# Optimization experiments

Measured on AMD Instinct MI355X. Metric: run time of the kernel, lower is better.

Reference implementation:

```python
import jax, jax.numpy as jnp
import numpy as np
import math

EPS = 1e-5
HEADS = 8

def _lin(x, w, b):
    return x @ w.T + b

def _ln(x, g, b):
    m = x.mean(-1, keepdims=True)
    v = ((x - m) ** 2).mean(-1, keepdims=True)
    return (x - m) / jnp.sqrt(v + EPS) * g + b

def _bn_eval(x, g, b):
    # BatchNorm1d eval with init running stats (mean=0, var=1)
    return x / jnp.sqrt(1.0 + EPS) * g[None, :, None] + b[None, :, None]

def _conv1d(x, w, b, pad):
    y = jax.lax.conv_general_dilated(x, w, (1,), [(pad, pad)],
                                     dimension_numbers=('NCH', 'OIH', 'NCH'))
    return y + b[None, :, None]

def _interp_linear(x, out_len):
    # F.interpolate(mode='linear', align_corners=False) on last axis
    L = x.shape[-1]
    src = (jnp.arange(out_len) + 0.5) * (L / out_len) - 0.5
    src = jnp.clip(src, 0.0, L - 1)
    i0 = jnp.floor(src).astype(jnp.int32)
    i1 = jnp.minimum(i0 + 1, L - 1)
    w = (src - i0).astype(x.dtype)
    return x[..., i0] * (1.0 - w) + x[..., i1] * w

def setup_inputs():
    key = jax.random.key(0)
    ks = iter(jax.random.split(key, 64))
    def nrm(shape, scale=0.02):
        return jax.random.normal(next(ks), shape, dtype=jnp.float32) * scale
    B, T, N, H, HOR, C = 2, 64, 2048, 128, 24, 32
    return dict(
        x=jax.random.normal(next(ks), (B, T, N), dtype=jnp.float32),
        tc_w=nrm((C, 1, 3), 0.2), tc_b=jnp.zeros((C,)), tc_bn_g=jnp.ones((C,)), tc_bn_b=jnp.zeros((C,)),
        fp_w=nrm((H, C * T)), fp_b=jnp.zeros((H,)), fp_ln_g=jnp.ones((H,)), fp_ln_b=jnp.zeros((H,)),
        q_w=nrm((H, H)), q_b=jnp.zeros((H,)),
        k_w=nrm((H, H)), k_b=jnp.zeros((H,)),
        v_w=nrm((H, H)), v_b=jnp.zeros((H,)),
        o_w=nrm((H, H)), o_b=jnp.zeros((H,)),
        adj=nrm((1, HEADS, N, N), 0.02),
        s0_w=nrm((H, H, 1), 0.05), s0_b=jnp.zeros((H,)), s0_bn_g=jnp.ones((H,)), s0_bn_b=jnp.zeros((H,)),
        s1_w=nrm((H, H, 2), 0.05), s1_b=jnp.zeros((H,)), s1_bn_g=jnp.ones((H,)), s1_bn_b=jnp.zeros((H,)),
        fusion_weight=jnp.ones((2,)),
        fu_w=nrm((H, H)), fu_b=jnp.zeros((H,)), fu_ln_g=jnp.ones((H,)), fu_ln_b=jnp.zeros((H,)),
        pr1_w=nrm((H, H)), pr1_b=jnp.zeros((H,)), pr_ln_g=jnp.ones((H,)), pr_ln_b=jnp.zeros((H,)),
        pr2_w=nrm((HOR, H)), pr2_b=jnp.zeros((HOR,)),
        rg_w=nrm((HOR, H)), rg_b=jnp.zeros((HOR,)),
    )

def _forward(x, tc_w, tc_b, tc_bn_g, tc_bn_b, fp_w, fp_b, fp_ln_g, fp_ln_b,
             q_w, q_b, k_w, k_b, v_w, v_b, o_w, o_b, adj,
             s0_w, s0_b, s0_bn_g, s0_bn_b, s1_w, s1_b, s1_bn_g, s1_bn_b,
             fusion_weight, fu_w, fu_b, fu_ln_g, fu_ln_b,
             pr1_w, pr1_b, pr_ln_g, pr_ln_b, pr2_w, pr2_b, rg_w, rg_b):
    B, T, N = x.shape
    H = q_w.shape[0]
    hd = H // HEADS
    x_last = x[:, -1, :]                                  # (B, N)
    # temporal conv over the window per node
    xt = x.transpose(0, 2, 1).reshape(B * N, 1, T)
    f = jax.nn.relu(_bn_eval(_conv1d(xt, tc_w, tc_b, 1), tc_bn_g, tc_bn_b))
    f = f.reshape(B, N, -1)                               # (B, N, 32*T)
    feats = jax.nn.relu(_ln(_lin(f, fp_w, fp_b), fp_ln_g, fp_ln_b))
    # adaptive graph attention with learnable adjacency bias
    q = _lin(feats, q_w, q_b).reshape(B, N, HEADS, hd)
    k = _lin(feats, k_w, k_b).reshape(B, N, HEADS, hd)
    v = _lin(feats, v_w, v_b).reshape(B, N, HEADS, hd)
    scores = jnp.einsum('bnhd,bmhd->bhnm', q, k) / math.sqrt(hd) + adj
    attn = jax.nn.softmax(scores, axis=-1)                # (B, HEADS, N, N)
    reg = jnp.float32(1e-4) * jnp.mean(jnp.abs(attn))
    go = jnp.einsum('bhnm,bmhd->bnhd', attn, v).reshape(B, N, H)
    gf = _lin(go, o_w, o_b)                               # (B, N, H)
    # multi-scale fusion (conv over node axis, kernels 1 and 2)
    xc = gf.transpose(0, 2, 1)                            # (B, H, N)
    f0 = jax.nn.relu(_bn_eval(_conv1d(xc, s0_w, s0_b, 0), s0_bn_g, s0_bn_b))
    f1 = jax.nn.relu(_bn_eval(_conv1d(xc, s1_w, s1_b, 1), s1_bn_g, s1_bn_b))  # (B,H,N+1)
    f1 = _interp_linear(f1, N)
    alpha = jax.nn.softmax(fusion_weight)
    fused = (alpha[0] * f0 + alpha[1] * f1).transpose(0, 2, 1)
    ff = jax.nn.relu(_ln(_lin(fused, fu_w, fu_b), fu_ln_g, fu_ln_b))
    # progressive prediction refinement
    h = jax.nn.relu(_ln(_lin(ff, pr1_w, pr1_b), pr_ln_g, pr_ln_b))
    preds = _lin(h, pr2_w, pr2_b)                         # (B, N, horizon)
    gates = jax.nn.sigmoid(_lin(ff, rg_w, rg_b))
    refined = gates * x_last[..., None] + (1.0 - gates) * preds
    return refined.transpose(0, 2, 1), reg                # (B, horizon, N), scalar

def reference(x, tc_w, tc_b, tc_bn_g, tc_bn_b, fp_w, fp_b, fp_ln_g, fp_ln_b,
              q_w, q_b, k_w, k_b, v_w, v_b, o_w, o_b, adj,
              s0_w, s0_b, s0_bn_g, s0_bn_b, s1_w, s1_b, s1_bn_g, s1_bn_b,
              fusion_weight, fu_w, fu_b, fu_ln_g, fu_ln_b,
              pr1_w, pr1_b, pr_ln_g, pr_ln_b, pr2_w, pr2_b, rg_w, rg_b):
    return _forward(x, tc_w, tc_b, tc_bn_g, tc_bn_b, fp_w, fp_b, fp_ln_g, fp_ln_b,
                    q_w, q_b, k_w, k_b, v_w, v_b, o_w, o_b, adj,
                    s0_w, s0_b, s0_bn_g, s0_bn_b, s1_w, s1_b, s1_bn_g, s1_bn_b,
                    fusion_weight, fu_w, fu_b, fu_ln_g, fu_ln_b,
                    pr1_w, pr1_b, pr_ln_g, pr_ln_b, pr2_w, pr2_b, rg_w, rg_b)
```

## Files before the change

### kernel.cpp

```cpp
#include <hip/hip_runtime.h>

using f32x4  = __attribute__((ext_vector_type(4))) float;
using bf16x8 = __attribute__((ext_vector_type(8))) short;

#define DEV static __device__ __forceinline__

DEV unsigned short f2bf(float f){
  unsigned u = __float_as_uint(f);
  unsigned r = (u + 0x7FFFu + ((u >> 16) & 1u)) >> 16;
  return (unsigned short)r;
}

__global__ __launch_bounds__(256) void prep_conv_kernel(
    const float* __restrict__ fp_w, const float* __restrict__ q_w,
    const float* __restrict__ k_w, const float* __restrict__ v_w,
    const float* __restrict__ o_w, const float* __restrict__ s0_w,
    const float* __restrict__ s1_w, const float* __restrict__ fu_w,
    const float* __restrict__ pr1_w, const float* __restrict__ pr2_w,
    const float* __restrict__ rg_w,
    unsigned short* __restrict__ fpw_bf, unsigned short* __restrict__ wcat_bf,
    float* __restrict__ o_wT, float* __restrict__ fu_wT, float* __restrict__ pr1_wT,
    float* __restrict__ s0_wT, float* __restrict__ s1_wT0, float* __restrict__ s1_wT1,
    float* __restrict__ pr2_wT, float* __restrict__ rg_wT,
    const float* __restrict__ x, const float* __restrict__ tc_w,
    const float* __restrict__ tc_b, const float* __restrict__ bn_g,
    const float* __restrict__ bn_b, unsigned short* __restrict__ f){
  if (blockIdx.x < 512){
    int i = blockIdx.x * 256 + threadIdx.x;
    const int stride = 512 * 256;
    for (int idx = i; idx < 128 * 2048; idx += stride) fpw_bf[idx] = f2bf(fp_w[idx]);
    for (int idx = i; idx < 384 * 128; idx += stride){
      int c = idx >> 7, k = idx & 127;
      float v;
      if (c < 128)      v = q_w[c * 128 + k] * 0.25f;
      else if (c < 256) v = k_w[(c - 128) * 128 + k];
      else              v = v_w[(c - 256) * 128 + k];
      wcat_bf[idx] = f2bf(v);
    }
    for (int idx = i; idx < 128 * 128; idx += stride){
      int k = idx >> 7, c = idx & 127;
      o_wT[idx]   = o_w[c * 128 + k];
      fu_wT[idx]  = fu_w[c * 128 + k];
      pr1_wT[idx] = pr1_w[c * 128 + k];
      s0_wT[idx]  = s0_w[c * 128 + k];
      s1_wT0[idx] = s1_w[(c * 128 + k) * 2 + 0];
      s1_wT1[idx] = s1_w[(c * 128 + k) * 2 + 1];
    }
    for (int idx = i; idx < 128 * 24; idx += stride){
      int k = idx / 24, c = idx % 24;
      pr2_wT[idx] = pr2_w[c * 128 + k];
      rg_wT[idx]  = rg_w[c * 128 + k];
    }
  } else {
    int lane = threadIdx.x & 63;
    int w = threadIdx.x >> 6;
    int row = (blockIdx.x - 512) * 4 + w;
    int b = row >> 11, n = row & 2047;
    float xv = x[(size_t)(b * 64 + lane) * 2048 + n];
    float xm = __shfl_up(xv, 1, 64);   if (lane == 0)  xm = 0.f;
    float xp = __shfl_down(xv, 1, 64); if (lane == 63) xp = 0.f;
    const float inv = rsqrtf(1.0f + 1e-5f);
    unsigned short* frow = f + (size_t)row * 2048;
    #pragma unroll
    for (int c = 0; c < 32; c++){
      float y = xm * tc_w[c * 3 + 0] + xv * tc_w[c * 3 + 1] + xp * tc_w[c * 3 + 2] + tc_b[c];
      y = y * inv * bn_g[c] + bn_b[c];
      frow[c * 64 + lane] = f2bf(fmaxf(y, 0.f));
    }
  }
}

__global__ __launch_bounds__(512) void feat_kernel(
    const unsigned short* __restrict__ f, const unsigned short* __restrict__ fpw,
    const float* __restrict__ fp_b, const float* __restrict__ ln_g,
    const float* __restrict__ ln_b, unsigned short* __restrict__ feats){
  __shared__ float pre[16][128];
  __shared__ float stat[16][2];
  int t = threadIdx.x;
  int lane = t & 63, w = t >> 6;
  int l15 = lane & 15, g = lane >> 4;
  int row0 = blockIdx.x * 16;
  int c0 = w * 16;
  f32x4 acc = {0.f,0.f,0.f,0.f};
  const unsigned short* arow = f   + (size_t)(row0 + l15) * 2048 + g * 8;
  const unsigned short* bp   = fpw + (size_t)(c0 + l15) * 2048 + g * 8;
  #pragma unroll 4
  for (int k = 0; k < 2048; k += 32){
    bf16x8 a  = *(const bf16x8*)(arow + k);
    bf16x8 b0 = *(const bf16x8*)(bp + k);
    acc = __builtin_amdgcn_mfma_f32_16x16x32_bf16(a, b0, acc, 0, 0, 0);
  }
  #pragma unroll
  for (int r = 0; r < 4; r++)
    pre[g * 4 + r][c0 + l15] = acc[r] + fp_b[c0 + l15];
  __syncthreads();
  if (t < 256){
    int r = t >> 4, j = t & 15;
    float s = 0.f, ss = 0.f;
    #pragma unroll
    for (int q = 0; q < 8; q++){ float v = pre[r][j + q * 16]; s += v; ss += v * v; }
    #pragma unroll
    for (int m = 1; m < 16; m <<= 1){ s += __shfl_xor(s, m, 64); ss += __shfl_xor(ss, m, 64); }
    if (j == 0){
      float mean = s * (1.f / 128.f);
      stat[r][0] = mean;
      stat[r][1] = rsqrtf(ss * (1.f / 128.f) - mean * mean + 1e-5f);
    }
  }
  __syncthreads();
  if (t < 256){
    int r = t >> 4, j = t & 15;
    float mean = stat[r][0], rstd = stat[r][1];
    bf16x8 outv;
    #pragma unroll
    for (int q = 0; q < 8; q++){
      int c = j * 8 + q;
      float v = (pre[r][c] - mean) * rstd * ln_g[c] + ln_b[c];
      outv[q] = (short)f2bf(fmaxf(v, 0.f));
    }
    *(bf16x8*)(feats + (size_t)(row0 + r) * 128 + j * 8) = outv;
  }
}

__global__ __launch_bounds__(256) void qkv_kernel(
    const unsigned short* __restrict__ feats, const unsigned short* __restrict__ wcat,
    const float* __restrict__ q_b, const float* __restrict__ k_b,
    const float* __restrict__ v_b, unsigned short* __restrict__ qo,
    unsigned short* __restrict__ ko, unsigned short* __restrict__ vT){
  int t = threadIdx.x, lane = t & 63, w = t >> 6;
  int l15 = lane & 15, g = lane >> 4;
  int row0 = blockIdx.x * 16;
  int c0 = w * 96;
  f32x4 acc[6];
  #pragma unroll
  for (int i = 0; i < 6; i++) acc[i] = (f32x4){0.f,0.f,0.f,0.f};
  const unsigned short* arow = feats + (size_t)(row0 + l15) * 128 + g * 8;
  #pragma unroll
  for (int k = 0; k < 128; k += 32){
    bf16x8 a = *(const bf16x8*)(arow + k);
    #pragma unroll
    for (int ni = 0; ni < 6; ni++){
      bf16x8 bb = *(const bf16x8*)(wcat + (size_t)(c0 + ni * 16 + l15) * 128 + g * 8 + k);
      acc[ni] = __builtin_amdgcn_mfma_f32_16x16x32_bf16(a, bb, acc[ni], 0, 0, 0);
    }
  }
  #pragma unroll
  for (int ni = 0; ni < 6; ni++){
    int c = c0 + ni * 16 + l15;
    int mat = c >> 7, cm = c & 127;
    int h = cm >> 4, d = cm & 15;
    float bias = (mat == 0) ? q_b[cm] * 0.25f : (mat == 1 ? k_b[cm] : v_b[cm]);
    #pragma unroll
    for (int r = 0; r < 4; r++){
      int row = row0 + g * 4 + r;
      int b = row >> 11, n = row & 2047;
      unsigned short bv = f2bf(acc[ni][r] + bias);
      int bh = b * 8 + h;
      if (mat == 0)      qo[((size_t)bh * 2048 + n) * 16 + d] = bv;
      else if (mat == 1) ko[((size_t)bh * 2048 + n) * 16 + d] = bv;
      else               vT[((size_t)bh * 16 + d) * 2048 + n] = bv;
    }
  }
}

__global__ __launch_bounds__(256) void attn_kernel(
    const unsigned short* __restrict__ qo, const unsigned short* __restrict__ ko,
    const unsigned short* __restrict__ vT, const float* __restrict__ adj,
    float* __restrict__ go){
  __shared__ unsigned short Pls[4][1024];
  __shared__ float adjs[4][16][68];
  __shared__ float red_acc[4][2][16][16];
  __shared__ float red_rs[4][2][16];
  int t = threadIdx.x, lane = t & 63, w = t >> 6;
  int l15 = lane & 15, g = lane >> 4;
  int h = blockIdx.x >> 7;
  int row0 = (blockIdx.x & 127) * 16;
  const bf16x8 zf = {0,0,0,0,0,0,0,0};
  bf16x8 qf[2];
  #pragma unroll
  for (int b = 0; b < 2; b++){
    if (g < 2) qf[b] = *(const bf16x8*)(qo + ((size_t)(b * 8 + h) * 2048 + row0 + l15) * 16 + g * 8);
    else       qf[b] = zf;
  }
  f32x4 accv[2] = {{0.f,0.f,0.f,0.f},{0.f,0.f,0.f,0.f}};
  float rs[2][4] = {{0,0,0,0},{0,0,0,0}};
  const float* adjbase = adj + ((size_t)h * 2048 + row0) * 2048;
  unsigned short* P = Pls[w];
  float (*A)[68] = adjs[w];
  const int mbeg = w * 512;
  for (int m0 = mbeg; m0 < mbeg + 512; m0 += 64){
    #pragma unroll
    for (int it = 0; it < 4; it++){
      int idx = it * 64 + lane;
      int rr = idx >> 4, c4 = (idx & 15) << 2;
      *(f32x4*)(&A[rr][c4]) = *(const f32x4*)(adjbase + (size_t)rr * 2048 + m0 + c4);
    }
    #pragma unroll
    for (int b = 0; b < 2; b++){
      int bh = b * 8 + h;
      const unsigned short* kbase = ko + (size_t)bh * 2048 * 16;
      f32x4 sf[4];
      #pragma unroll
      for (int s = 0; s < 4; s++){
        bf16x8 kf;
        if (g < 2) kf = *(const bf16x8*)(kbase + (size_t)(m0 + s * 16 + l15) * 16 + g * 8);
        else       kf = zf;
        f32x4 z4 = {0.f,0.f,0.f,0.f};
        sf[s] = __builtin_amdgcn_mfma_f32_16x16x32_bf16(qf[b], kf, z4, 0, 0, 0);
      }
      #pragma unroll
      for (int s = 0; s < 4; s++){
        #pragma unroll
        for (int r = 0; r < 4; r++){
          int rowl = g * 4 + r;
          float p = __expf(sf[s][r] + A[rowl][s * 16 + l15]);
          rs[b][r] += p;
          int col = s * 16 + l15;
          int chunk = col >> 3;
          P[rowl * 64 + (((chunk ^ (rowl & 7)) << 3) | (col & 7))] = f2bf(p);
        }
      }
      const unsigned short* vbase = vT + (size_t)bh * 16 * 2048;
      #pragma unroll
      for (int half = 0; half < 2; half++){
        int chunk = half * 4 + g;
        bf16x8 af = *(const bf16x8*)(P + l15 * 64 + ((chunk ^ (l15 & 7)) << 3));
        bf16x8 vf = *(const bf16x8*)(vbase + (size_t)l15 * 2048 + m0 + half * 32 + g * 8);
        accv[b] = __builtin_amdgcn_mfma_f32_16x16x32_bf16(af, vf, accv[b], 0, 0, 0);
      }
    }
  }
  #pragma unroll
  for (int b = 0; b < 2; b++){
    #pragma unroll
    for (int r = 0; r < 4; r++){
      float s = rs[b][r];
      #pragma unroll
      for (int m = 1; m < 16; m <<= 1) s += __shfl_xor(s, m, 64);
      red_acc[w][b][g * 4 + r][l15] = accv[b][r];
      if (l15 == 0) red_rs[w][b][g * 4 + r] = s;
    }
  }
  __syncthreads();
  for (int i = t; i < 512; i += 256){
    int b = i >> 8, row = (i >> 4) & 15, col = i & 15;
    float v = 0.f, d = 0.f;
    #pragma unroll
    for (int ww = 0; ww < 4; ww++){ v += red_acc[ww][b][row][col]; d += red_rs[ww][b][row]; }
    go[((size_t)b * 2048 + row0 + row) * 128 + h * 16 + col] = v / d;
  }
}

__global__ __launch_bounds__(512) void tail_kernel(
    const float* __restrict__ go, const float* __restrict__ x,
    const float* __restrict__ o_wT, const float* __restrict__ o_b,
    const float* __restrict__ s0_wT, const float* __restrict__ s0_b,
    const float* __restrict__ s0_g, const float* __restrict__ s0_bb,
    const float* __restrict__ s1_wT0, const float* __restrict__ s1_wT1,
    const float* __restrict__ s1_b, const float* __restrict__ s1_g,
    const float* __restrict__ s1_bb, const float* __restrict__ fw,
    const float* __restrict__ fu_wT, const float* __restrict__ fu_b,
    const float* __restrict__ fu_g, const float* __restrict__ fu_bb,
    const float* __restrict__ pr1_wT, const float* __restrict__ pr1_b,
    const float* __restrict__ pr_g, const float* __restrict__ pr_bb,
    const float* __restrict__ pr2_wT, const float* __restrict__ pr2_b,
    const float* __restrict__ rg_wT, const float* __restrict__ rg_b,
    float* __restrict__ out){
  __shared__ float go_s[20][128];
  __shared__ float gf_s[21][128];
  __shared__ float f1_s[17][128];
  __shared__ float fu_in[16][128];
  __shared__ float pre_s[16][128];
  __shared__ float ff_s[16][128];
  __shared__ float h_s[16][128];
  __shared__ float stat[16][2];
  int t = threadIdx.x;
  int b = blockIdx.x >> 7;
  int n0 = (blockIdx.x & 127) * 16;
  for (int e = t; e < 20 * 128; e += 512){
    int lr = e >> 7, cc = e & 127;
    int gn = n0 - 1 + lr;
    go_s[lr][cc] = (lr < 18 && gn >= 0 && gn < 2048) ? go[((size_t)b * 2048 + gn) * 128 + cc] : 0.f;
  }
  __syncthreads();
  int c = t & 127, q4 = t >> 7;
  const float bninv = rsqrtf(1.0f + 1e-5f);
  {
    float acc[5];
    float bias = o_b[c];
    #pragma unroll
    for (int i = 0; i < 5; i++) acc[i] = bias;
    for (int k = 0; k < 128; k++){
      float wv = o_wT[k * 128 + c];
      #pragma unroll
      for (int i = 0; i < 5; i++) acc[i] += go_s[i * 4 + q4][k] * wv;
    }
    #pragma unroll
    for (int i = 0; i < 5; i++){
      int lr = i * 4 + q4;
      int gn = n0 - 1 + lr;
      gf_s[lr][c] = (lr < 18 && gn >= 0 && gn < 2048) ? acc[i] : 0.f;
    }
    if (t < 128) gf_s[20][t] = 0.f;
  }
  __syncthreads();
  {
    float acc[5];
    float bias = s1_b[c];
    #pragma unroll
    for (int i = 0; i < 5; i++) acc[i] = bias;
    for (int k = 0; k < 128; k++){
      float w0 = s1_wT0[k * 128 + c], w1 = s1_wT1[k * 128 + c];
      #pragma unroll
      for (int i = 0; i < 5; i++)
        acc[i] += gf_s[i * 4 + q4][k] * w0 + gf_s[i * 4 + q4 + 1][k] * w1;
    }
    float sc = s1_g[c] * bninv, bb2 = s1_bb[c];
    #pragma unroll
    for (int i = 0; i < 5; i++){
      int lr = i * 4 + q4;
      if (lr < 17) f1_s[lr][c] = fmaxf(acc[i] * sc + bb2, 0.f);
    }
  }
  __syncthreads();
  {
    float acc[4];
    float bias = s0_b[c];
    #pragma unroll
    for (int i = 0; i < 4; i++) acc[i] = bias;
    for (int k = 0; k < 128; k++){
      float wv = s0_wT[k * 128 + c];
      #pragma unroll
      for (int i = 0; i < 4; i++) acc[i] += gf_s[i * 4 + q4 + 1][k] * wv;
    }
    float e0 = __expf(fw[0]), e1 = __expf(fw[1]);
    float a0 = e0 / (e0 + e1), a1 = e1 / (e0 + e1);
    float sc = s0_g[c] * bninv, bb2 = s0_bb[c];
    #pragma unroll
    for (int i = 0; i < 4; i++){
      int lr = i * 4 + q4;
      int n = n0 + lr;
      float f0 = fmaxf(acc[i] * sc + bb2, 0.f);
      float wn = (n + 0.5f) * (1.0f / 2048.0f);
      fu_in[lr][c] = a0 * f0 + a1 * ((1.f - wn) * f1_s[lr][c] + wn * f1_s[lr + 1][c]);
    }
  }
  __syncthreads();
  {
    float acc[4];
    float bias = fu_b[c];
    #pragma unroll
    for (int i = 0; i < 4; i++) acc[i] = bias;
    for (int k = 0; k < 128; k++){
      float wv = fu_wT[k * 128 + c];
      #pragma unroll
      for (int i = 0; i < 4; i++) acc[i] += fu_in[i * 4 + q4][k] * wv;
    }
    #pragma unroll
    for (int i = 0; i < 4; i++) pre_s[i * 4 + q4][c] = acc[i];
  }
  __syncthreads();
  if (t < 256){
    int r = t >> 4, j = t & 15;
    float s = 0.f, ss = 0.f;
    #pragma unroll
    for (int q = 0; q < 8; q++){ float v = pre_s[r][j + q * 16]; s += v; ss += v * v; }
    #pragma unroll
    for (int m = 1; m < 16; m <<= 1){ s += __shfl_xor(s, m, 64); ss += __shfl_xor(ss, m, 64); }
    if (j == 0){ float mean = s * (1.f / 128.f); stat[r][0] = mean;
                 stat[r][1] = rsqrtf(ss * (1.f / 128.f) - mean * mean + 1e-5f); }
  }
  __syncthreads();
  if (t < 256){
    int r = t >> 4, j = t & 15;
    float mean = stat[r][0], rstd = stat[r][1];
    #pragma unroll
    for (int q = 0; q < 8; q++){
      int cc = j * 8 + q;
      ff_s[r][cc] = fmaxf((pre_s[r][cc] - mean) * rstd * fu_g[cc] + fu_bb[cc], 0.f);
    }
  }
  __syncthreads();
  {
    float acc[4];
    float bias = pr1_b[c];
    #pragma unroll
    for (int i = 0; i < 4; i++) acc[i] = bias;
    for (int k = 0; k < 128; k++){
      float wv = pr1_wT[k * 128 + c];
      #pragma unroll
      for (int i = 0; i < 4; i++) acc[i] += ff_s[i * 4 + q4][k] * wv;
    }
    #pragma unroll
    for (int i = 0; i < 4; i++) pre_s[i * 4 + q4][c] = acc[i];
  }
  __syncthreads();
  if (t < 256){
    int r = t >> 4, j = t & 15;
    float s = 0.f, ss = 0.f;
    #pragma unroll
    for (int q = 0; q < 8; q++){ float v = pre_s[r][j + q * 16]; s += v; ss += v * v; }
    #pragma unroll
    for (int m = 1; m < 16; m <<= 1){ s += __shfl_xor(s, m, 64); ss += __shfl_xor(ss, m, 64); }
    if (j == 0){ float mean = s * (1.f / 128.f); stat[r][0] = mean;
                 stat[r][1] = rsqrtf(ss * (1.f / 128.f) - mean * mean + 1e-5f); }
  }
  __syncthreads();
  if (t < 256){
    int r = t >> 4, j = t & 15;
    float mean = stat[r][0], rstd = stat[r][1];
    #pragma unroll
    for (int q = 0; q < 8; q++){
      int cc = j * 8 + q;
      h_s[r][cc] = fmaxf((pre_s[r][cc] - mean) * rstd * pr_g[cc] + pr_bb[cc], 0.f);
    }
  }
  __syncthreads();
  if (t < 384){
    int lr = t / 24, cc = t % 24;
    float accp = pr2_b[cc], accg = rg_b[cc];
    for (int k = 0; k < 128; k++){
      accp += h_s[lr][k] * pr2_wT[k * 24 + cc];
      accg += ff_s[lr][k] * rg_wT[k * 24 + cc];
    }
    float gate = 1.f / (1.f + __expf(-accg));
    int n = n0 + lr;
    float xl = x[((size_t)b * 64 + 63) * 2048 + n];
    out[((size_t)b * 24 + cc) * 2048 + n] = gate * xl + (1.f - gate) * accp;
  }
  if (blockIdx.x == 0 && t == 0) out[2 * 24 * 2048] = 1e-4f / 2048.0f;
}

extern "C" void kernel_launch(void* const* d_in, const int* in_sizes, int n_in,
                              void* d_out, int out_size, void* d_ws, size_t ws_size,
                              hipStream_t stream){
  const float* x       = (const float*)d_in[0];
  const float* tc_w    = (const float*)d_in[1];
  const float* tc_b    = (const float*)d_in[2];
  const float* tc_bn_g = (const float*)d_in[3];
  const float* tc_bn_b = (const float*)d_in[4];
  const float* fp_w    = (const float*)d_in[5];
  const float* fp_b    = (const float*)d_in[6];
  const float* fp_ln_g = (const float*)d_in[7];
  const float* fp_ln_b = (const float*)d_in[8];
  const float* q_w     = (const float*)d_in[9];
  const float* q_b     = (const float*)d_in[10];
  const float* k_w     = (const float*)d_in[11];
  const float* k_b     = (const float*)d_in[12];
  const float* v_w     = (const float*)d_in[13];
  const float* v_b     = (const float*)d_in[14];
  const float* o_w     = (const float*)d_in[15];
  const float* o_b     = (const float*)d_in[16];
  const float* adj     = (const float*)d_in[17];
  const float* s0_w    = (const float*)d_in[18];
  const float* s0_b    = (const float*)d_in[19];
  const float* s0_bn_g = (const float*)d_in[20];
  const float* s0_bn_b = (const float*)d_in[21];
  const float* s1_w    = (const float*)d_in[22];
  const float* s1_b    = (const float*)d_in[23];
  const float* s1_bn_g = (const float*)d_in[24];
  const float* s1_bn_b = (const float*)d_in[25];
  const float* fusion_w= (const float*)d_in[26];
  const float* fu_w    = (const float*)d_in[27];
  const float* fu_b    = (const float*)d_in[28];
  const float* fu_ln_g = (const float*)d_in[29];
  const float* fu_ln_b = (const float*)d_in[30];
  const float* pr1_w   = (const float*)d_in[31];
  const float* pr1_b   = (const float*)d_in[32];
  const float* pr_ln_g = (const float*)d_in[33];
  const float* pr_ln_b = (const float*)d_in[34];
  const float* pr2_w   = (const float*)d_in[35];
  const float* pr2_b   = (const float*)d_in[36];
  const float* rg_w    = (const float*)d_in[37];
  const float* rg_b    = (const float*)d_in[38];
  float* out = (float*)d_out;

  char* ws = (char*)d_ws;
  size_t off = 0;
  auto alloc = [&](size_t bytes) -> void* {
    void* p = ws + off;
    off += (bytes + 255) & ~(size_t)255;
    return p;
  };
  unsigned short* f_bf    = (unsigned short*)alloc((size_t)4096 * 2048 * 2);
  unsigned short* fpw_bf  = (unsigned short*)alloc((size_t)128 * 2048 * 2);
  unsigned short* wcat_bf = (unsigned short*)alloc((size_t)384 * 128 * 2);
  unsigned short* feats_bf= (unsigned short*)alloc((size_t)4096 * 128 * 2);
  unsigned short* q_bf    = (unsigned short*)alloc((size_t)16 * 2048 * 16 * 2);
  unsigned short* k_bf    = (unsigned short*)alloc((size_t)16 * 2048 * 16 * 2);
  unsigned short* vT_bf   = (unsigned short*)alloc((size_t)16 * 2048 * 16 * 2);
  float* go     = (float*)alloc((size_t)4096 * 128 * 4);
  float* o_wT   = (float*)alloc(128 * 128 * 4);
  float* fu_wT  = (float*)alloc(128 * 128 * 4);
  float* pr1_wT = (float*)alloc(128 * 128 * 4);
  float* s0_wT  = (float*)alloc(128 * 128 * 4);
  float* s1_wT0 = (float*)alloc(128 * 128 * 4);
  float* s1_wT1 = (float*)alloc(128 * 128 * 4);
  float* pr2_wT = (float*)alloc(128 * 24 * 4);
  float* rg_wT  = (float*)alloc(128 * 24 * 4);
  if (off > ws_size) return;

  prep_conv_kernel<<<1536, 256, 0, stream>>>(fp_w, q_w, k_w, v_w, o_w, s0_w, s1_w,
                                             fu_w, pr1_w, pr2_w, rg_w, fpw_bf, wcat_bf,
                                             o_wT, fu_wT, pr1_wT, s0_wT, s1_wT0, s1_wT1,
                                             pr2_wT, rg_wT,
                                             x, tc_w, tc_b, tc_bn_g, tc_bn_b, f_bf);
  feat_kernel<<<256, 512, 0, stream>>>(f_bf, fpw_bf, fp_b, fp_ln_g, fp_ln_b, feats_bf);
  qkv_kernel<<<256, 256, 0, stream>>>(feats_bf, wcat_bf, q_b, k_b, v_b, q_bf, k_bf, vT_bf);
  attn_kernel<<<1024, 256, 0, stream>>>(q_bf, k_bf, vT_bf, adj, go);
  tail_kernel<<<256, 512, 0, stream>>>(go, x, o_wT, o_b, s0_wT, s0_b, s0_bn_g, s0_bn_b,
                                       s1_wT0, s1_wT1, s1_b, s1_bn_g, s1_bn_b, fusion_w,
                                       fu_wT, fu_b, fu_ln_g, fu_ln_b, pr1_wT, pr1_b,
                                       pr_ln_g, pr_ln_b, pr2_wT, pr2_b, rg_wT, rg_b, out);
}
```

Before: 138.2 us.

## Fuse conv, feature projection and QKV; register-resident attention P; widen tail

Merges the temporal conv, the feature projection GEMM with LayerNorm, and the QKV projection into one kernel that builds the conv output in swizzled shared memory. This removes the large bf16 conv intermediate and the feats round trip through global memory. The attention kernel swaps MFMA operand order so the softmax probabilities stay in registers as the B operand, and it loads adj directly into registers with V stored in a permuted layout. The tail kernel moves to 1024 threads with fewer rows per thread. Risks include lower occupancy from the large shared footprint and serialized conv compute inside the fused kernel.

```diff
diff --git a/kernel.cpp b/kernel.cpp
--- a/kernel.cpp
+++ b/kernel.cpp
@@ -11,7 +11,11 @@
   return (unsigned short)r;
 }
 
-__global__ __launch_bounds__(256) void prep_conv_kernel(
+DEV int vperm(int n){
+  return (n & ~63) | (n & 32) | ((n & 0xC) << 1) | ((n & 0x10) >> 2) | (n & 3);
+}
+
+__global__ __launch_bounds__(256) void prep_kernel(
     const float* __restrict__ fp_w, const float* __restrict__ q_w,
     const float* __restrict__ k_w, const float* __restrict__ v_w,
     const float* __restrict__ o_w, const float* __restrict__ s0_w,
@@ -21,78 +25,97 @@
     unsigned short* __restrict__ fpw_bf, unsigned short* __restrict__ wcat_bf,
     float* __restrict__ o_wT, float* __restrict__ fu_wT, float* __restrict__ pr1_wT,
     float* __restrict__ s0_wT, float* __restrict__ s1_wT0, float* __restrict__ s1_wT1,
-    float* __restrict__ pr2_wT, float* __restrict__ rg_wT,
+    float* __restrict__ pr2_wT, float* __restrict__ rg_wT){
+  int i = blockIdx.x * 256 + threadIdx.x;
+  const int stride = 128 * 256;
+  for (int idx = i; idx < 128 * 2048; idx += stride) fpw_bf[idx] = f2bf(fp_w[idx]);
+  for (int idx = i; idx < 384 * 128; idx += stride){
+    int c = idx >> 7, k = idx & 127;
+    float v;
+    if (c < 128)      v = q_w[c * 128 + k] * 0.25f;
+    else if (c < 256) v = k_w[(c - 128) * 128 + k];
+    else              v = v_w[(c - 256) * 128 + k];
+    wcat_bf[idx] = f2bf(v);
+  }
+  for (int idx = i; idx < 128 * 128; idx += stride){
+    int k = idx >> 7, c = idx & 127;
+    o_wT[idx]   = o_w[c * 128 + k];
+    fu_wT[idx]  = fu_w[c * 128 + k];
+    pr1_wT[idx] = pr1_w[c * 128 + k];
+    s0_wT[idx]  = s0_w[c * 128 + k];
+    s1_wT0[idx] = s1_w[(c * 128 + k) * 2 + 0];
+    s1_wT1[idx] = s1_w[(c * 128 + k) * 2 + 1];
+  }
+  for (int idx = i; idx < 128 * 24; idx += stride){
+    int k = idx / 24, c = idx % 24;
+    pr2_wT[idx] = pr2_w[c * 128 + k];
+    rg_wT[idx]  = rg_w[c * 128 + k];
+  }
+}
+
+__global__ __launch_bounds__(512) void fused_feat_kernel(
     const float* __restrict__ x, const float* __restrict__ tc_w,
     const float* __restrict__ tc_b, const float* __restrict__ bn_g,
-    const float* __restrict__ bn_b, unsigned short* __restrict__ f){
-  if (blockIdx.x < 512){
-    int i = blockIdx.x * 256 + threadIdx.x;
-    const int stride = 512 * 256;
-    for (int idx = i; idx < 128 * 2048; idx += stride) fpw_bf[idx] = f2bf(fp_w[idx]);
-    for (int idx = i; idx < 384 * 128; idx += stride){
-      int c = idx >> 7, k = idx & 127;
-      float v;
-      if (c < 128)      v = q_w[c * 128 + k] * 0.25f;
-      else if (c < 256) v = k_w[(c - 128) * 128 + k];
-      else              v = v_w[(c - 256) * 128 + k];
-      wcat_bf[idx] = f2bf(v);
-    }
-    for (int idx = i; idx < 128 * 128; idx += stride){
-      int k = idx >> 7, c = idx & 127;
-      o_wT[idx]   = o_w[c * 128 + k];
-      fu_wT[idx]  = fu_w[c * 128 + k];
-      pr1_wT[idx] = pr1_w[c * 128 + k];
-      s0_wT[idx]  = s0_w[c * 128 + k];
-      s1_wT0[idx] = s1_w[(c * 128 + k) * 2 + 0];
-      s1_wT1[idx] = s1_w[(c * 128 + k) * 2 + 1];
-    }
-    for (int idx = i; idx < 128 * 24; idx += stride){
-      int k = idx / 24, c = idx % 24;
-      pr2_wT[idx] = pr2_w[c * 128 + k];
-      rg_wT[idx]  = rg_w[c * 128 + k];
-    }
-  } else {
-    int lane = threadIdx.x & 63;
-    int w = threadIdx.x >> 6;
-    int row = (blockIdx.x - 512) * 4 + w;
-    int b = row >> 11, n = row & 2047;
-    float xv = x[(size_t)(b * 64 + lane) * 2048 + n];
-    float xm = __shfl_up(xv, 1, 64);   if (lane == 0)  xm = 0.f;
-    float xp = __shfl_down(xv, 1, 64); if (lane == 63) xp = 0.f;
-    const float inv = rsqrtf(1.0f + 1e-5f);
-    unsigned short* frow = f + (size_t)row * 2048;
-    #pragma unroll
-    for (int c = 0; c < 32; c++){
-      float y = xm * tc_w[c * 3 + 0] + xv * tc_w[c * 3 + 1] + xp * tc_w[c * 3 + 2] + tc_b[c];
-      y = y * inv * bn_g[c] + bn_b[c];
-      frow[c * 64 + lane] = f2bf(fmaxf(y, 0.f));
-    }
-  }
-}
-
-__global__ __launch_bounds__(512) void feat_kernel(
-    const unsigned short* __restrict__ f, const unsigned short* __restrict__ fpw,
-    const float* __restrict__ fp_b, const float* __restrict__ ln_g,
-    const float* __restrict__ ln_b, unsigned short* __restrict__ feats){
+    const float* __restrict__ bn_b,
+    const unsigned short* __restrict__ fpw, const float* __restrict__ fp_b,
+    const float* __restrict__ ln_g, const float* __restrict__ ln_b,
+    const unsigned short* __restrict__ wcat, const float* __restrict__ q_b,
+    const float* __restrict__ k_b, const float* __restrict__ v_b,
+    unsigned short* __restrict__ qo, unsigned short* __restrict__ ko,
+    unsigned short* __restrict__ vTp){
+  __shared__ float xs[64][17];
+  __shared__ unsigned short fs[16 * 1024];
   __shared__ float pre[16][128];
+  __shared__ unsigned short ft[16 * 128];
   __shared__ float stat[16][2];
   int t = threadIdx.x;
-  int lane = t & 63, w = t >> 6;
-  int l15 = lane & 15, g = lane >> 4;
+  int lane = t & 63, w = t >> 6, l15 = lane & 15, g = lane >> 4;
   int row0 = blockIdx.x * 16;
-  int c0 = w * 16;
-  f32x4 acc = {0.f,0.f,0.f,0.f};
-  const unsigned short* arow = f   + (size_t)(row0 + l15) * 2048 + g * 8;
-  const unsigned short* bp   = fpw + (size_t)(c0 + l15) * 2048 + g * 8;
-  #pragma unroll 4
-  for (int k = 0; k < 2048; k += 32){
-    bf16x8 a  = *(const bf16x8*)(arow + k);
-    bf16x8 b0 = *(const bf16x8*)(bp + k);
-    acc = __builtin_amdgcn_mfma_f32_16x16x32_bf16(a, b0, acc, 0, 0, 0);
-  }
-  #pragma unroll
-  for (int r = 0; r < 4; r++)
-    pre[g * 4 + r][c0 + l15] = acc[r] + fp_b[c0 + l15];
+  int b = row0 >> 11, n0 = row0 & 2047;
+  for (int e = t; e < 1024; e += 512){
+    int tt = e >> 4, nn2 = e & 15;
+    xs[tt][nn2] = x[(size_t)(b * 64 + tt) * 2048 + n0 + nn2];
+  }
+  int nn = t & 15, ch = t >> 4;
+  float cw0 = tc_w[ch * 3 + 0], cw1 = tc_w[ch * 3 + 1], cw2 = tc_w[ch * 3 + 2];
+  float cbias = tc_b[ch];
+  float cbnsc = rsqrtf(1.0f + 1e-5f) * bn_g[ch];
+  float cbnb  = bn_b[ch];
+  int toff = (ch & 3) << 4;
+  f32x4 acc = {0.f, 0.f, 0.f, 0.f};
+  const unsigned short* bp = fpw + (size_t)(w * 16 + l15) * 2048 + g * 8;
+  __syncthreads();
+  for (int half = 0; half < 2; half++){
+    if ((ch >> 4) == half){
+      int cl = ch & 15;
+      #pragma unroll
+      for (int i = 0; i < 64; i++){
+        int tt = (i + toff) & 63;
+        float xm = (tt > 0)  ? xs[tt - 1][nn] : 0.f;
+        float xv = xs[tt][nn];
+        float xp = (tt < 63) ? xs[tt + 1][nn] : 0.f;
+        float y = (xm * cw0 + xv * cw1 + xp * cw2 + cbias) * cbnsc + cbnb;
+        int kl = cl * 64 + tt;
+        int byte = nn * 2048 + ((kl * 2) ^ ((nn & 7) << 4));
+        *(unsigned short*)((char*)fs + byte) = f2bf(fmaxf(y, 0.f));
+      }
+    }
+    __syncthreads();
+    #pragma unroll 4
+    for (int kk = 0; kk < 1024; kk += 32){
+      int abyte = l15 * 2048 + (((kk + g * 8) * 2) ^ ((l15 & 7) << 4));
+      bf16x8 a  = *(const bf16x8*)((const char*)fs + abyte);
+      bf16x8 bb = *(const bf16x8*)(bp + half * 1024 + kk);
+      acc = __builtin_amdgcn_mfma_f32_16x16x32_bf16(a, bb, acc, 0, 0, 0);
+    }
+    __syncthreads();
+  }
+  {
+    int c0 = w * 16;
+    #pragma unroll
+    for (int r = 0; r < 4; r++)
+      pre[g * 4 + r][c0 + l15] = acc[r] + fp_b[c0 + l15];
+  }
   __syncthreads();
   if (t < 256){
     int r = t >> 4, j = t & 15;
@@ -114,61 +137,48 @@
     bf16x8 outv;
     #pragma unroll
     for (int q = 0; q < 8; q++){
-      int c = j * 8 + q;
-      float v = (pre[r][c] - mean) * rstd * ln_g[c] + ln_b[c];
+      int cc = j * 8 + q;
+      float v = (pre[r][cc] - mean) * rstd * ln_g[cc] + ln_b[cc];
       outv[q] = (short)f2bf(fmaxf(v, 0.f));
     }
-    *(bf16x8*)(feats + (size_t)(row0 + r) * 128 + j * 8) = outv;
-  }
-}
-
-__global__ __launch_bounds__(256) void qkv_kernel(
-    const unsigned short* __restrict__ feats, const unsigned short* __restrict__ wcat,
-    const float* __restrict__ q_b, const float* __restrict__ k_b,
-    const float* __restrict__ v_b, unsigned short* __restrict__ qo,
-    unsigned short* __restrict__ ko, unsigned short* __restrict__ vT){
-  int t = threadIdx.x, lane = t & 63, w = t >> 6;
-  int l15 = lane & 15, g = lane >> 4;
-  int row0 = blockIdx.x * 16;
-  int c0 = w * 96;
-  f32x4 acc[6];
+    int byte = r * 256 + ((j * 16) ^ ((r & 7) << 4));
+    *(bf16x8*)((char*)ft + byte) = outv;
+  }
+  __syncthreads();
+  f32x4 acc3[3] = {{0,0,0,0},{0,0,0,0},{0,0,0,0}};
   #pragma unroll
-  for (int i = 0; i < 6; i++) acc[i] = (f32x4){0.f,0.f,0.f,0.f};
-  const unsigned short* arow = feats + (size_t)(row0 + l15) * 128 + g * 8;
+  for (int kk = 0; kk < 128; kk += 32){
+    int abyte = l15 * 256 + (((kk + g * 8) * 2) ^ ((l15 & 7) << 4));
+    bf16x8 a = *(const bf16x8*)((const char*)ft + abyte);
+    #pragma unroll
+    for (int ci = 0; ci < 3; ci++){
+      int c0 = w * 48 + ci * 16;
+      bf16x8 bb = *(const bf16x8*)(wcat + (size_t)(c0 + l15) * 128 + g * 8 + kk);
+      acc3[ci] = __builtin_amdgcn_mfma_f32_16x16x32_bf16(a, bb, acc3[ci], 0, 0, 0);
+    }
+  }
   #pragma unroll
-  for (int k = 0; k < 128; k += 32){
-    bf16x8 a = *(const bf16x8*)(arow + k);
-    #pragma unroll
-    for (int ni = 0; ni < 6; ni++){
-      bf16x8 bb = *(const bf16x8*)(wcat + (size_t)(c0 + ni * 16 + l15) * 128 + g * 8 + k);
-      acc[ni] = __builtin_amdgcn_mfma_f32_16x16x32_bf16(a, bb, acc[ni], 0, 0, 0);
-    }
-  }
-  #pragma unroll
-  for (int ni = 0; ni < 6; ni++){
-    int c = c0 + ni * 16 + l15;
+  for (int ci = 0; ci < 3; ci++){
+    int c = w * 48 + ci * 16 + l15;
     int mat = c >> 7, cm = c & 127;
-    int h = cm >> 4, d = cm & 15;
+    int hh = cm >> 4, d = cm & 15;
     float bias = (mat == 0) ? q_b[cm] * 0.25f : (mat == 1 ? k_b[cm] : v_b[cm]);
+    int bh = b * 8 + hh;
     #pragma unroll
     for (int r = 0; r < 4; r++){
-      int row = row0 + g * 4 + r;
-      int b = row >> 11, n = row & 2047;
-      unsigned short bv = f2bf(acc[ni][r] + bias);
-      int bh = b * 8 + h;
+      int n = n0 + g * 4 + r;
+      unsigned short bv = f2bf(acc3[ci][r] + bias);
       if (mat == 0)      qo[((size_t)bh * 2048 + n) * 16 + d] = bv;
       else if (mat == 1) ko[((size_t)bh * 2048 + n) * 16 + d] = bv;
-      else               vT[((size_t)bh * 16 + d) * 2048 + n] = bv;
+      else               vTp[((size_t)bh * 16 + d) * 2048 + vperm(n)] = bv;
     }
   }
 }
 
 __global__ __launch_bounds__(256) void attn_kernel(
     const unsigned short* __restrict__ qo, const unsigned short* __restrict__ ko,
-    const unsigned short* __restrict__ vT, const float* __restrict__ adj,
+    const unsigned short* __restrict__ vTp, const float* __restrict__ adj,
     float* __restrict__ go){
-  __shared__ unsigned short Pls[4][1024];
-  __shared__ float adjs[4][16][68];
   __shared__ float red_acc[4][2][16][16];
   __shared__ float red_rs[4][2][16];
   int t = threadIdx.x, lane = t & 63, w = t >> 6;
@@ -176,6 +186,7 @@
   int h = blockIdx.x >> 7;
   int row0 = (blockIdx.x & 127) * 16;
   const bf16x8 zf = {0,0,0,0,0,0,0,0};
+  const f32x4 z4 = {0.f,0.f,0.f,0.f};
   bf16x8 qf[2];
   #pragma unroll
   for (int b = 0; b < 2; b++){
@@ -183,18 +194,14 @@
     else       qf[b] = zf;
   }
   f32x4 accv[2] = {{0.f,0.f,0.f,0.f},{0.f,0.f,0.f,0.f}};
-  float rs[2][4] = {{0,0,0,0},{0,0,0,0}};
-  const float* adjbase = adj + ((size_t)h * 2048 + row0) * 2048;
-  unsigned short* P = Pls[w];
-  float (*A)[68] = adjs[w];
+  float rsp[2] = {0.f, 0.f};
+  const float* adjrow = adj + ((size_t)h * 2048 + row0 + l15) * 2048 + g * 4;
   const int mbeg = w * 512;
   for (int m0 = mbeg; m0 < mbeg + 512; m0 += 64){
-    #pragma unroll
-    for (int it = 0; it < 4; it++){
-      int idx = it * 64 + lane;
-      int rr = idx >> 4, c4 = (idx & 15) << 2;
-      *(f32x4*)(&A[rr][c4]) = *(const f32x4*)(adjbase + (size_t)rr * 2048 + m0 + c4);
-    }
+    f32x4 adjv[4];
+    #pragma unroll
+    for (int s = 0; s < 4; s++)
+      adjv[s] = *(const f32x4*)(adjrow + m0 + s * 16);
     #pragma unroll
     for (int b = 0; b < 2; b++){
       int bh = b * 8 + h;
@@ -205,53 +212,48 @@
         bf16x8 kf;
         if (g < 2) kf = *(const bf16x8*)(kbase + (size_t)(m0 + s * 16 + l15) * 16 + g * 8);
         else       kf = zf;
-        f32x4 z4 = {0.f,0.f,0.f,0.f};
-        sf[s] = __builtin_amdgcn_mfma_f32_16x16x32_bf16(qf[b], kf, z4, 0, 0, 0);
+        sf[s] = __builtin_amdgcn_mfma_f32_16x16x32_bf16(kf, qf[b], z4, 0, 0, 0);
       }
+      bf16x8 pf[2];
+      float partial = 0.f;
       #pragma unroll
       for (int s = 0; s < 4; s++){
         #pragma unroll
         for (int r = 0; r < 4; r++){
-          int rowl = g * 4 + r;
-          float p = __expf(sf[s][r] + A[rowl][s * 16 + l15]);
-          rs[b][r] += p;
-          int col = s * 16 + l15;
-          int chunk = col >> 3;
-          P[rowl * 64 + (((chunk ^ (rowl & 7)) << 3) | (col & 7))] = f2bf(p);
+          float p = __expf(sf[s][r] + adjv[s][r]);
+          partial += p;
+          pf[s >> 1][(s & 1) * 4 + r] = (short)f2bf(p);
         }
       }
-      const unsigned short* vbase = vT + (size_t)bh * 16 * 2048;
+      rsp[b] += partial;
+      const unsigned short* vbase = vTp + ((size_t)bh * 16 + l15) * 2048 + m0;
       #pragma unroll
-      for (int half = 0; half < 2; half++){
-        int chunk = half * 4 + g;
-        bf16x8 af = *(const bf16x8*)(P + l15 * 64 + ((chunk ^ (l15 & 7)) << 3));
-        bf16x8 vf = *(const bf16x8*)(vbase + (size_t)l15 * 2048 + m0 + half * 32 + g * 8);
-        accv[b] = __builtin_amdgcn_mfma_f32_16x16x32_bf16(af, vf, accv[b], 0, 0, 0);
+      for (int h2 = 0; h2 < 2; h2++){
+        bf16x8 vf = *(const bf16x8*)(vbase + h2 * 32 + g * 8);
+        accv[b] = __builtin_amdgcn_mfma_f32_16x16x32_bf16(vf, pf[h2], accv[b], 0, 0, 0);
       }
     }
   }
   #pragma unroll
   for (int b = 0; b < 2; b++){
-    #pragma unroll
-    for (int r = 0; r < 4; r++){
-      float s = rs[b][r];
-      #pragma unroll
-      for (int m = 1; m < 16; m <<= 1) s += __shfl_xor(s, m, 64);
-      red_acc[w][b][g * 4 + r][l15] = accv[b][r];
-      if (l15 == 0) red_rs[w][b][g * 4 + r] = s;
-    }
+    float s = rsp[b];
+    s += __shfl_xor(s, 16, 64);
+    s += __shfl_xor(s, 32, 64);
+    #pragma unroll
+    for (int r = 0; r < 4; r++) red_acc[w][b][g * 4 + r][l15] = accv[b][r];
+    if (lane < 16) red_rs[w][b][l15] = s;
   }
   __syncthreads();
   for (int i = t; i < 512; i += 256){
-    int b = i >> 8, row = (i >> 4) & 15, col = i & 15;
-    float v = 0.f, d = 0.f;
-    #pragma unroll
-    for (int ww = 0; ww < 4; ww++){ v += red_acc[ww][b][row][col]; d += red_rs[ww][b][row]; }
-    go[((size_t)b * 2048 + row0 + row) * 128 + h * 16 + col] = v / d;
-  }
-}
-
-__global__ __launch_bounds__(512) void tail_kernel(
+    int b = i >> 8, q = (i >> 4) & 15, d = i & 15;
+    float v = 0.f, den = 0.f;
+    #pragma unroll
+    for (int ww = 0; ww < 4; ww++){ v += red_acc[ww][b][d][q]; den += red_rs[ww][b][q]; }
+    go[((size_t)b * 2048 + row0 + q) * 128 + h * 16 + d] = v / den;
+  }
+}
+
+__global__ __launch_bounds__(1024) void tail_kernel(
     const float* __restrict__ go, const float* __restrict__ x,
     const float* __restrict__ o_wT, const float* __restrict__ o_b,
     const float* __restrict__ s0_wT, const float* __restrict__ s0_b,
@@ -266,8 +268,8 @@
     const float* __restrict__ pr2_wT, const float* __restrict__ pr2_b,
     const float* __restrict__ rg_wT, const float* __restrict__ rg_b,
     float* __restrict__ out){
-  __shared__ float go_s[20][128];
-  __shared__ float gf_s[21][128];
+  __shared__ float go_s[18][128];
+  __shared__ float gf_s[18][128];
   __shared__ float f1_s[17][128];
   __shared__ float fu_in[16][128];
   __shared__ float pre_s[16][128];
@@ -277,87 +279,76 @@
   int t = threadIdx.x;
   int b = blockIdx.x >> 7;
   int n0 = (blockIdx.x & 127) * 16;
-  for (int e = t; e < 20 * 128; e += 512){
+  for (int e = t; e < 18 * 128; e += 1024){
     int lr = e >> 7, cc = e & 127;
     int gn = n0 - 1 + lr;
-    go_s[lr][cc] = (lr < 18 && gn >= 0 && gn < 2048) ? go[((size_t)b * 2048 + gn) * 128 + cc] : 0.f;
-  }
-  __syncthreads();
-  int c = t & 127, q4 = t >> 7;
+    go_s[lr][cc] = (gn >= 0 && gn < 2048) ? go[((size_t)b * 2048 + gn) * 128 + cc] : 0.f;
+  }
+  __syncthreads();
+  int c = t & 127, q8 = t >> 7;
   const float bninv = rsqrtf(1.0f + 1e-5f);
   {
-    float acc[5];
     float bias = o_b[c];
-    #pragma unroll
-    for (int i = 0; i < 5; i++) acc[i] = bias;
+    float a0 = bias, a1 = bias, a2 = bias;
     for (int k = 0; k < 128; k++){
       float wv = o_wT[k * 128 + c];
-      #pragma unroll
-      for (int i = 0; i < 5; i++) acc[i] += go_s[i * 4 + q4][k] * wv;
-    }
-    #pragma unroll
-    for (int i = 0; i < 5; i++){
-      int lr = i * 4 + q4;
-      int gn = n0 - 1 + lr;
-      gf_s[lr][c] = (lr < 18 && gn >= 0 && gn < 2048) ? acc[i] : 0.f;
-    }
-    if (t < 128) gf_s[20][t] = 0.f;
+      a0 += go_s[q8][k] * wv;
+      a1 += go_s[q8 + 8][k] * wv;
+      if (q8 < 2) a2 += go_s[q8 + 16][k] * wv;
+    }
+    int gn = n0 - 1 + q8;
+    gf_s[q8][c]      = (gn >= 0 && gn < 2048) ? a0 : 0.f;
+    gf_s[q8 + 8][c]  = (gn + 8 < 2048) ? a1 : 0.f;
+    if (q8 < 2) gf_s[q8 + 16][c] = (gn + 16 < 2048) ? a2 : 0.f;
   }
   __syncthreads();
   {
-    float acc[5];
     float bias = s1_b[c];
-    #pragma unroll
-    for (int i = 0; i < 5; i++) acc[i] = bias;
+    float a0 = bias, a1 = bias, a2 = bias;
     for (int k = 0; k < 128; k++){
       float w0 = s1_wT0[k * 128 + c], w1 = s1_wT1[k * 128 + c];
-      #pragma unroll
-      for (int i = 0; i < 5; i++)
-        acc[i] += gf_s[i * 4 + q4][k] * w0 + gf_s[i * 4 + q4 + 1][k] * w1;
+      a0 += gf_s[q8][k] * w0 + gf_s[q8 + 1][k] * w1;
+      a1 += gf_s[q8 + 8][k] * w0 + gf_s[q8 + 9][k] * w1;
+      if (q8 == 0) a2 += gf_s[16][k] * w0 + gf_s[17][k] * w1;
     }
     float sc = s1_g[c] * bninv, bb2 = s1_bb[c];
-    #pragma unroll
-    for (int i = 0; i < 5; i++){
-      int lr = i * 4 + q4;
-      if (lr < 17) f1_s[lr][c] = fmaxf(acc[i] * sc + bb2, 0.f);
-    }
+    f1_s[q8][c]     = fmaxf(a0 * sc + bb2, 0.f);
+    f1_s[q8 + 8][c] = fmaxf(a1 * sc + bb2, 0.f);
+    if (q8 == 0) f1_s[16][c] = fmaxf(a2 * sc + bb2, 0.f);
   }
   __syncthreads();
   {
-    float acc[4];
     float bias = s0_b[c];
-    #pragma unroll
-    for (int i = 0; i < 4; i++) acc[i] = bias;
+    float a0 = bias, a1 = bias;
     for (int k = 0; k < 128; k++){
       float wv = s0_wT[k * 128 + c];
-      #pragma unroll
-      for (int i = 0; i < 4; i++) acc[i] += gf_s[i * 4 + q4 + 1][k] * wv;
+      a0 += gf_s[q8 + 1][k] * wv;
+      a1 += gf_s[q8 + 9][k] * wv;
     }
     float e0 = __expf(fw[0]), e1 = __expf(fw[1]);
-    float a0 = e0 / (e0 + e1), a1 = e1 / (e0 + e1);
+    float al0 = e0 / (e0 + e1), al1 = e1 / (e0 + e1);
     float sc = s0_g[c] * bninv, bb2 = s0_bb[c];
     #pragma unroll
-    for (int i = 0; i < 4; i++){
-      int lr = i * 4 + q4;
+    for (int i = 0; i < 2; i++){
+      int lr = q8 + i * 8;
+      float accv = i ? a1 : a0;
       int n = n0 + lr;
-      float f0 = fmaxf(acc[i] * sc + bb2, 0.f);
+      float f0 = fmaxf(accv * sc + bb2, 0.f);
       float wn = (n + 0.5f) * (1.0f / 2048.0f);
-      fu_in[lr][c] = a0 * f0 + a1 * ((1.f - wn) * f1_s[lr][c] + wn * f1_s[lr + 1][c]);
+      fu_in[lr][c] = al0 * f0 + al1 * ((1.f - wn) * f1_s[lr][c] + wn * f1_s[lr + 1][c]);
     }
   }
   __syncthreads();
   {
-    float acc[4];
     float bias = fu_b[c];
-    #pragma unroll
-    for (int i = 0; i < 4; i++) acc[i] = bias;
+    float a0 = bias, a1 = bias;
     for (int k = 0; k < 128; k++){
       float wv = fu_wT[k * 128 + c];
-      #pragma unroll
-      for (int i = 0; i < 4; i++) acc[i] += fu_in[i * 4 + q4][k] * wv;
-    }
-    #pragma unroll
-    for (int i = 0; i < 4; i++) pre_s[i * 4 + q4][c] = acc[i];
+      a0 += fu_in[q8][k] * wv;
+      a1 += fu_in[q8 + 8][k] * wv;
+    }
+    pre_s[q8][c] = a0;
+    pre_s[q8 + 8][c] = a1;
   }
   __syncthreads();
   if (t < 256){
@@ -382,17 +373,15 @@
   }
   __syncthreads();
   {
-    float acc[4];
     float bias = pr1_b[c];
-    #pragma unroll
-    for (int i = 0; i < 4; i++) acc[i] = bias;
+    float a0 = bias, a1 = bias;
     for (int k = 0; k < 128; k++){
       float wv = pr1_wT[k * 128 + c];
-      #pragma unroll
-      for (int i = 0; i < 4; i++) acc[i] += ff_s[i * 4 + q4][k] * wv;
-    }
-    #pragma unroll
-    for (int i = 0; i < 4; i++) pre_s[i * 4 + q4][c] = acc[i];
+      a0 += ff_s[q8][k] * wv;
+      a1 += ff_s[q8 + 8][k] * wv;
+    }
+    pre_s[q8][c] = a0;
+    pre_s[q8 + 8][c] = a1;
   }
   __syncthreads();
   if (t < 256){
@@ -482,13 +471,11 @@
     off += (bytes + 255) & ~(size_t)255;
     return p;
   };
-  unsigned short* f_bf    = (unsigned short*)alloc((size_t)4096 * 2048 * 2);
   unsigned short* fpw_bf  = (unsigned short*)alloc((size_t)128 * 2048 * 2);
   unsigned short* wcat_bf = (unsigned short*)alloc((size_t)384 * 128 * 2);
-  unsigned short* feats_bf= (unsigned short*)alloc((size_t)4096 * 128 * 2);
   unsigned short* q_bf    = (unsigned short*)alloc((size_t)16 * 2048 * 16 * 2);
   unsigned short* k_bf    = (unsigned short*)alloc((size_t)16 * 2048 * 16 * 2);
-  unsigned short* vT_bf   = (unsigned short*)alloc((size_t)16 * 2048 * 16 * 2);
+  unsigned short* vTp_bf  = (unsigned short*)alloc((size_t)16 * 2048 * 16 * 2);
   float* go     = (float*)alloc((size_t)4096 * 128 * 4);
   float* o_wT   = (float*)alloc(128 * 128 * 4);
   float* fu_wT  = (float*)alloc(128 * 128 * 4);
@@ -500,16 +487,17 @@
   float* rg_wT  = (float*)alloc(128 * 24 * 4);
   if (off > ws_size) return;
 
-  prep_conv_kernel<<<1536, 256, 0, stream>>>(fp_w, q_w, k_w, v_w, o_w, s0_w, s1_w,
-                                             fu_w, pr1_w, pr2_w, rg_w, fpw_bf, wcat_bf,
-                                             o_wT, fu_wT, pr1_wT, s0_wT, s1_wT0, s1_wT1,
-                                             pr2_wT, rg_wT,
-                                             x, tc_w, tc_b, tc_bn_g, tc_bn_b, f_bf);
-  feat_kernel<<<256, 512, 0, stream>>>(f_bf, fpw_bf, fp_b, fp_ln_g, fp_ln_b, feats_bf);
-  qkv_kernel<<<256, 256, 0, stream>>>(feats_bf, wcat_bf, q_b, k_b, v_b, q_bf, k_bf, vT_bf);
-  attn_kernel<<<1024, 256, 0, stream>>>(q_bf, k_bf, vT_bf, adj, go);
-  tail_kernel<<<256, 512, 0, stream>>>(go, x, o_wT, o_b, s0_wT, s0_b, s0_bn_g, s0_bn_b,
-                                       s1_wT0, s1_wT1, s1_b, s1_bn_g, s1_bn_b, fusion_w,
-                                       fu_wT, fu_b, fu_ln_g, fu_ln_b, pr1_wT, pr1_b,
-                                       pr_ln_g, pr_ln_b, pr2_wT, pr2_b, rg_wT, rg_b, out);
-}
+  prep_kernel<<<128, 256, 0, stream>>>(fp_w, q_w, k_w, v_w, o_w, s0_w, s1_w,
+                                       fu_w, pr1_w, pr2_w, rg_w, fpw_bf, wcat_bf,
+                                       o_wT, fu_wT, pr1_wT, s0_wT, s1_wT0, s1_wT1,
+                                       pr2_wT, rg_wT);
+  fused_feat_kernel<<<256, 512, 0, stream>>>(x, tc_w, tc_b, tc_bn_g, tc_bn_b,
+                                             fpw_bf, fp_b, fp_ln_g, fp_ln_b,
+                                             wcat_bf, q_b, k_b, v_b,
+                                             q_bf, k_bf, vTp_bf);
+  attn_kernel<<<1024, 256, 0, stream>>>(q_bf, k_bf, vTp_bf, adj, go);
+  tail_kernel<<<256, 1024, 0, stream>>>(go, x, o_wT, o_b, s0_wT, s0_b, s0_bn_g, s0_bn_b,
+                                        s1_wT0, s1_wT1, s1_b, s1_bn_g, s1_bn_b, fusion_w,
+                                        fu_wT, fu_b, fu_ln_g, fu_ln_b, pr1_wT, pr1_b,
+                                        pr_ln_g, pr_ln_b, pr2_wT, pr2_b, rg_wT, rg_b, out);
+}
```

Result: slower. 145.2 us (+5.1%).
